# Optimization experiments

Measured on AMD Instinct MI355X. Metric: run time of the kernel, lower is better.

Reference implementation:

```python
import jax, jax.numpy as jnp
import numpy as np
from jax import lax

CORRKS = 7
EPS_CORR = 1e-6
EPS_IN = 1e-5
FLOW_SCALE = 1.0


def _gauss_kernel2d():
    # kornia get_gaussian_kernel1d(7, 1.5), separable -> outer product
    x = np.arange(7, dtype=np.float32) - 3.0
    g = np.exp(-(x ** 2) / (2.0 * 1.5 ** 2))
    g = g / g.sum()
    return jnp.asarray(np.outer(g, g), dtype=jnp.float32)  # [7,7]


def conv2d(x, w, b=None, padding=1, dilation=1, groups=1):
    y = lax.conv_general_dilated(
        x, w, window_strides=(1, 1),
        padding=[(padding, padding), (padding, padding)],
        rhs_dilation=(dilation, dilation),
        dimension_numbers=("NCHW", "OIHW", "NCHW"),
        feature_group_count=groups)
    if b is not None:
        y = y + b[None, :, None, None]
    return y


def gaussian_blur(x):
    # replicate padding then depthwise 7x7 gaussian conv
    c = x.shape[1]
    k2 = _gauss_kernel2d()
    w = jnp.broadcast_to(k2[None, None], (c, 1, 7, 7))
    xp = jnp.pad(x, ((0, 0), (0, 0), (3, 3), (3, 3)), mode="edge")
    return conv2d(xp, w, padding=0, groups=c)


def instance_norm(x, gamma, beta):
    mu = x.mean(axis=(2, 3), keepdims=True)
    var = x.var(axis=(2, 3), keepdims=True)
    xn = (x - mu) * lax.rsqrt(var + EPS_IN)
    return xn * gamma[None, :, None, None] + beta[None, :, None, None]


def lrelu(x):
    return jnp.where(x >= 0, x, 0.2 * x)


def nan0(x):
    return jnp.nan_to_num(x, nan=0.0, posinf=0.0, neginf=0.0)


def setup_inputs() -> dict:
    key = jax.random.key(0)
    ks = jax.random.split(key, 20)
    b, c, h, w = 4, 64, 256, 256

    def rn(k, shape, scale):
        return jax.random.normal(k, shape, dtype=jnp.float32) * scale

    d = {}
    d["feat1"] = rn(ks[0], (b, c, h, w), 1.0)
    d["feat2"] = rn(ks[1], (b, c, h, w), 1.0)
    # preprocessor: Conv(c, c, 3, pad=1), bias, no norm/act
    d["pre_w"] = rn(ks[2], (c, c, 3, 3), 0.05)
    d["pre_b"] = jnp.zeros((c,), jnp.float32)
    # featcompressor layer1: Conv(2c,2c,3), IN affine + LeakyReLU (no bias)
    d["fc1_w"] = rn(ks[3], (2 * c, 2 * c, 3, 3), 0.05)
    d["fc1_g"] = jnp.ones((2 * c,), jnp.float32)
    d["fc1_be"] = jnp.zeros((2 * c,), jnp.float32)
    # featcompressor layer2: Conv(2c,c,3), bias, no norm/act
    d["fc2_w"] = rn(ks[4], (c, 2 * c, 3, 3), 0.05)
    d["fc2_b"] = jnp.zeros((c,), jnp.float32)
    # estimator: (c+49)->64 d1, 64->32 d2, 32->16 d4; IN + LeakyReLU, no bias
    d["e1_w"] = rn(ks[5], (64, c + CORRKS * CORRKS, 3, 3), 0.05)
    d["e1_g"] = jnp.ones((64,), jnp.float32)
    d["e1_be"] = jnp.zeros((64,), jnp.float32)
    d["e2_w"] = rn(ks[6], (32, 64, 3, 3), 0.05)
    d["e2_g"] = jnp.ones((32,), jnp.float32)
    d["e2_be"] = jnp.zeros((32,), jnp.float32)
    d["e3_w"] = rn(ks[7], (16, 32, 3, 3), 0.05)
    d["e3_g"] = jnp.ones((16,), jnp.float32)
    d["e3_be"] = jnp.zeros((16,), jnp.float32)
    # flow head (torch zero-inits; use small random so output is non-degenerate)
    d["head_w"] = rn(ks[8], (2, 16, 3, 3), 0.05)
    d["head_b"] = jnp.zeros((2,), jnp.float32)
    return d


def reference(feat1, feat2, pre_w, pre_b, fc1_w, fc1_g, fc1_be, fc2_w, fc2_b,
              e1_w, e1_g, e1_be, e2_w, e2_g, e2_be, e3_w, e3_g, e3_be,
              head_w, head_b):
    # preprocessor applied to both features (cat on batch == apply separately)
    f1 = conv2d(feat1, pre_w, pre_b, padding=1)
    f2 = conv2d(feat2, pre_w, pre_b, padding=1)

    # featcompressor
    feat = conv2d(jnp.concatenate([f1, f2], axis=1), fc1_w, padding=1)
    feat = lrelu(instance_norm(feat, fc1_g, fc1_be))
    feat = conv2d(feat, fc2_w, fc2_b, padding=1)

    # local correlation: (feat2 - shifted blurred feat1)^2 mean over channels
    b, c, h, w = f2.shape
    f1s = gaussian_blur(f1)
    pad = CORRKS // 2  # corr_dilation=1
    f1p = jnp.pad(f1s, ((0, 0), (0, 0), (pad, pad), (pad, pad)))  # zero pad (F.unfold)
    lc = jnp.stack(
        [((f2 - f1p[:, :, i:i + h, j:j + w]) ** 2).mean(axis=1)
         for i in range(CORRKS) for j in range(CORRKS)], axis=1)  # [b,49,h,w]
    lc = lc / (lc.mean(axis=(1, 2, 3), keepdims=True) + EPS_CORR)
    corr = nan0(jnp.concatenate([feat, lc], axis=1))  # [b, c+49, h, w]

    # dilated conv estimator stack
    x = lrelu(instance_norm(conv2d(corr, e1_w, padding=1, dilation=1), e1_g, e1_be))
    x = lrelu(instance_norm(conv2d(x, e2_w, padding=2, dilation=2), e2_g, e2_be))
    x = lrelu(instance_norm(conv2d(x, e3_w, padding=4, dilation=4), e3_g, e3_be))

    disp = conv2d(x, head_w, head_b, padding=1) * FLOW_SCALE
    disp = nan0(gaussian_blur(disp))
    return disp
```

## Files before the change

kernel.cpp:

```cpp
#include <hip/hip_runtime.h>
#include <hip/hip_bf16.h>


typedef __attribute__((ext_vector_type(8))) short short8;
typedef __attribute__((ext_vector_type(4))) float f32x4;
typedef _Float16 f16x8 __attribute__((ext_vector_type(8)));
typedef _Float16 f16x2 __attribute__((ext_vector_type(2)));

__device__ __forceinline__ float s2f(short s) {
    unsigned int u = ((unsigned int)(unsigned short)s) << 16;
    float f; __builtin_memcpy(&f, &u, 4); return f;
}
__device__ __forceinline__ short f2s(float f) {
    __hip_bfloat16 h = __float2bfloat16(f);
    short s; __builtin_memcpy(&s, &h, 2); return s;
}
__device__ __forceinline__ float h2f(short s) {
    _Float16 h; __builtin_memcpy(&h, &s, 2); return (float)h;
}
__device__ __forceinline__ short f2h(float f) {
    _Float16 h = (_Float16)f;
    short s; __builtin_memcpy(&s, &h, 2); return s;
}

__device__ __forceinline__ float gw(int j) {
    const float G[7] = {0.0366329f, 0.1112808f, 0.2167453f, 0.2706821f,
                        0.2167453f, 0.1112808f, 0.0366329f};
    return G[j];
}

__global__ __launch_bounds__(256) void transpose_k(const float* __restrict__ in,
                                                   short* __restrict__ out)
{
    __shared__ float t[64][65];
    const int b = blockIdx.y;
    const int px0 = blockIdx.x * 64;
    #pragma unroll
    for (int k = 0; k < 16; ++k) {
        int idx = threadIdx.x + k * 256;
        int c = idx >> 6, x = idx & 63;
        t[c][x] = in[(size_t)(b * 64 + c) * 65536 + px0 + x];
    }
    __syncthreads();
    #pragma unroll
    for (int k = 0; k < 16; ++k) {
        int idx = threadIdx.x + k * 256;
        int px = idx >> 6, c = idx & 63;
        out[(size_t)(b * 65536 + px0 + px) * 64 + c] = f2s(t[c][px]);
    }
}

__global__ __launch_bounds__(256) void repack2_k(const float* __restrict__ w,
                                                 short* __restrict__ o,
                                                 int cout, int cin, int CINP)
{
    int idx = blockIdx.x * 256 + threadIdx.x;
    int CB = CINP >> 5;
    int tot = cout * 9 * CINP;
    if (idx >= tot) return;
    int c8   = idx & 7;
    int lane = (idx >> 3) & 63;
    int rest = idx >> 9;
    int cb   = rest % CB;
    int rest2 = rest / CB;
    int tap  = rest2 % 9;
    int o16  = rest2 / 9;
    int n16 = lane & 15, q = lane >> 4;
    int oc = o16 * 16 + n16;
    int ic = cb * 32 + q * 8 + c8;
    float v = (ic < cin) ? w[(size_t)(oc * cin + ic) * 9 + tap] : 0.f;
    o[idx] = f2s(v);
}

template<int DIL, int CINP, int WX, int WY, int NOC, int G>
__global__ __launch_bounds__(256) void convmfma_k(
    const short* __restrict__ srcA, const short* __restrict__ srcB,
    int splitK, int csA, int csB,
    const short* __restrict__ wgt, const float* __restrict__ bias,
    short* __restrict__ out, int OSTR, int OBASE, int b0)
{
    static_assert(WX * WY == 4, "4 waves per block");
    constexpr int PXW = G * 16;
    constexpr int PXB = PXW * WX;
    constexpr int XT  = 256 / PXB;
    constexpr int CB  = CINP / 32;
    constexpr int UQ  = CINP / 8;
    constexpr int UPX = UQ + 1;
    constexpr int WPX = PXB + 2 * DIL;

    __shared__ __align__(16) short lds[WPX * UPX * 8];

    const int tid  = threadIdx.x;
    const int lane = tid & 63;
    const int wave = tid >> 6;
    const int q = lane >> 4, n16 = lane & 15;
    const int wx = wave % WX, wy = wave / WX;

    constexpr int NX = XT * 256;
    const int bx = blockIdx.x;
    const int xs = (bx & 7) * (NX >> 3) + (bx >> 3);
    const int xt = xs % XT;
    const int y  = xs / XT;

    const int b  = b0 + blockIdx.z;
    const int ocWaveBase = blockIdx.y * (16 * NOC * WY) + wy * (16 * NOC);
    const int o16base = ocWaveBase >> 4;
    const int x0 = xt * PXB + wx * PXW;
    const int gxbase = xt * PXB - DIL;

    f32x4 acc[G][NOC];
    #pragma unroll
    for (int g = 0; g < G; ++g)
        #pragma unroll
        for (int t = 0; t < NOC; ++t)
            acc[g][t] = {0.f, 0.f, 0.f, 0.f};

    for (int dyi = 0; dyi < 3; ++dyi) {
        const int yy = y + (dyi - 1) * DIL;
        const bool rowok = ((unsigned)yy < 256u);
        __syncthreads();
        if (rowok) {
            const int rowbase = (b * 256 + yy) * 256;
            for (int i = tid; i < WPX * UQ; i += 256) {
                const int pxl = i / UQ;
                const int u   = i - pxl * UQ;
                const int gx  = gxbase + pxl;
                short8 v = {0, 0, 0, 0, 0, 0, 0, 0};
                if ((unsigned)gx < 256u) {
                    const int ic = u * 8;
                    const short* p = (ic < splitK)
                        ? srcA + (size_t)(rowbase + gx) * csA + ic
                        : srcB + (size_t)(rowbase + gx) * csB + (ic - splitK);
                    v = *reinterpret_cast<const short8*>(p);
                }
                *reinterpret_cast<short8*>(&lds[(pxl * UPX + u) * 8]) = v;
            }
        }
        __syncthreads();
        if (!rowok) continue;

        #pragma unroll
        for (int dxi = 0; dxi < 3; ++dxi) {
            const int tap = dyi * 3 + dxi;
            #pragma unroll
            for (int cb = 0; cb < CB; ++cb) {
                short8 bfr[G];
                #pragma unroll
                for (int g = 0; g < G; ++g) {
                    const int pxl = wx * PXW + g * 16 + n16 + dxi * DIL;
                    bfr[g] = *reinterpret_cast<const short8*>(
                        &lds[(pxl * UPX + cb * 4 + q) * 8]);
                }
                #pragma unroll
                for (int t = 0; t < NOC; ++t) {
                    short8 a = *reinterpret_cast<const short8*>(
                        wgt + ((((size_t)(o16base + t) * 9 + tap) * CB + cb) * 64 + lane) * 8);
                    #pragma unroll
                    for (int g = 0; g < G; ++g)
                        acc[g][t] = __builtin_amdgcn_mfma_f32_16x16x32_bf16(
                            a, bfr[g], acc[g][t], 0, 0, 0);
                }
            }
        }
    }

    #pragma unroll
    for (int g = 0; g < G; ++g) {
        const size_t px_lin = (size_t)(b * 256 + y) * 256 + x0 + g * 16 + n16;
        #pragma unroll
        for (int t = 0; t < NOC; ++t) {
            const int oc = ocWaveBase + t * 16 + q * 4;
            f32x4 v = acc[g][t];
            if (bias) {
                v.x += bias[oc];     v.y += bias[oc + 1];
                v.z += bias[oc + 2]; v.w += bias[oc + 3];
            }
            ushort4 pk;
            pk.x = (unsigned short)f2s(v.x);
            pk.y = (unsigned short)f2s(v.y);
            pk.z = (unsigned short)f2s(v.z);
            pk.w = (unsigned short)f2s(v.w);
            *reinterpret_cast<ushort4*>(out + px_lin * OSTR + OBASE + oc) = pk;
        }
    }
}

__global__ __launch_bounds__(256) void in_stats_nhwc_k(const short* __restrict__ x,
                                                       float* __restrict__ sums,
                                                       int C, int lC)
{
    __shared__ float ls[256], lss[256];
    const int tid = threadIdx.x;
    const int b = blockIdx.y;
    const int c = tid & (C - 1);
    const int sub = tid >> lC;
    const int tpc = 256 >> lC;
    const int px0 = blockIdx.x * 512;
    float s = 0.f, ss = 0.f;
    for (int p = sub; p < 512; p += tpc) {
        float v = s2f(x[(size_t)(b * 65536 + px0 + p) * C + c]);
        s += v; ss += v * v;
    }
    ls[tid] = s; lss[tid] = ss;
    __syncthreads();
    if (tid < C) {
        float s0 = ls[tid], ss0 = lss[tid];
        for (int j = 1; j < tpc; ++j) { s0 += ls[tid + j * C]; ss0 += lss[tid + j * C]; }
        atomicAdd(sums + 2 * (b * C + tid), s0);
        atomicAdd(sums + 2 * (b * C + tid) + 1, ss0);
    }
}

__global__ __launch_bounds__(256) void in_finalize_k(const float* __restrict__ sums,
                                                     float* __restrict__ stats, int n)
{
    int i = blockIdx.x * 256 + threadIdx.x;
    if (i >= n) return;
    float m = sums[2 * i] * (1.f / 65536.f);
    float var = sums[2 * i + 1] * (1.f / 65536.f) - m * m;
    if (var < 0.f) var = 0.f;
    stats[2 * i] = m;
    stats[2 * i + 1] = rsqrtf(var + 1e-5f);
}

__global__ __launch_bounds__(256) void in_apply_nhwc_k(short* __restrict__ x,
                                                       const float* __restrict__ stats,
                                                       const float* __restrict__ gamma,
                                                       const float* __restrict__ beta,
                                                       int C, int lC, int n4)
{
    int i = blockIdx.x * 256 + threadIdx.x;
    if (i >= n4) return;
    int e0 = i * 4;
    int c0 = e0 & (C - 1);
    int b = e0 >> (16 + lC);
    ushort4 u = reinterpret_cast<ushort4*>(x)[i];
    unsigned short vs[4] = {u.x, u.y, u.z, u.w};
    #pragma unroll
    for (int j = 0; j < 4; ++j) {
        int bc = b * C + c0 + j;
        float t = (s2f((short)vs[j]) - stats[2 * bc]) * stats[2 * bc + 1]
                  * gamma[c0 + j] + beta[c0 + j];
        vs[j] = (unsigned short)f2s(t >= 0.f ? t : 0.2f * t);
    }
    u.x = vs[0]; u.y = vs[1]; u.z = vs[2]; u.w = vs[3];
    reinterpret_cast<ushort4*>(x)[i] = u;
}

__global__ __launch_bounds__(256) void blur_k(const short* __restrict__ A,
                                              short* __restrict__ B1)
{
    __shared__ __align__(16) short raw[484 * 8];
    __shared__ __align__(16) float hb[352 * 12];

    const int tid  = threadIdx.x;
    const int tile = blockIdx.x >> 3;
    const int g    = blockIdx.x & 7;
    const int c0   = g * 8;
    const int tx = (tile & 15) << 4;
    const int ty = (tile >> 4) << 4;
    const int b  = blockIdx.y;

    #pragma unroll
    for (int it = 0; it < 2; ++it) {
        int i = tid + it * 256;
        if (i < 484) {
            int y = i / 22, x = i - y * 22;
            int gy = ty + y - 3, gx = tx + x - 3;
            gy = gy < 0 ? 0 : (gy > 255 ? 255 : gy);
            gx = gx < 0 ? 0 : (gx > 255 ? 255 : gx);
            *reinterpret_cast<short8*>(&raw[i * 8]) =
                *reinterpret_cast<const short8*>(
                    &A[(size_t)((b << 16) + (gy << 8) + gx) * 128 + c0]);
        }
    }
    __syncthreads();

    #pragma unroll
    for (int it = 0; it < 2; ++it) {
        int i = tid + it * 256;
        if (i < 352) {
            int r = i >> 4, cc = i & 15;
            float s[8];
            #pragma unroll
            for (int c = 0; c < 8; ++c) s[c] = 0.f;
            #pragma unroll
            for (int j = 0; j < 7; ++j) {
                short8 v = *reinterpret_cast<const short8*>(&raw[(r * 22 + cc + j) * 8]);
                float w = gw(j);
                #pragma unroll
                for (int c = 0; c < 8; ++c) s[c] += w * s2f(v[c]);
            }
            #pragma unroll
            for (int c = 0; c < 8; ++c) hb[i * 12 + c] = s[c];
        }
    }
    __syncthreads();

    const int py = tid >> 4, px = tid & 15;
    float s[8];
    #pragma unroll
    for (int c = 0; c < 8; ++c) s[c] = 0.f;
    #pragma unroll
    for (int j = 0; j < 7; ++j) {
        const float* hp = &hb[((py + j) * 16 + px) * 12];
        float w = gw(j);
        #pragma unroll
        for (int c = 0; c < 8; ++c) s[c] += w * hp[c];
    }
    short8 ov;
    #pragma unroll
    for (int c = 0; c < 8; ++c) ov[c] = f2h(s[c]);
    *reinterpret_cast<short8*>(
        &B1[(size_t)(((g * 4 + b) << 16) + ((ty + py) << 8) + tx + px) * 8]) = ov;
}

__global__ __launch_bounds__(256, 2) void corr2_k(const short* __restrict__ A,
                                                  const short* __restrict__ B1,
                                                  short* __restrict__ lcPad,
                                                  float* __restrict__ lcsum)
{
    __shared__ __align__(16) short blh[2][484 * 8];
    __shared__ float red[4];

    const int tid = threadIdx.x;
    const int tx = (blockIdx.x & 15) << 4;
    const int ty = (blockIdx.x >> 4) << 4;
    const int b  = blockIdx.y;
    const int py = tid >> 4, px = tid & 15;

    int y0 = tid / 22, x0c = tid - y0 * 22;
    int gy0 = ty + y0 - 3, gx0 = tx + x0c - 3;
    const bool ok0 = (gy0 >= 0 && gy0 < 256 && gx0 >= 0 && gx0 < 256);
    gy0 = gy0 < 0 ? 0 : (gy0 > 255 ? 255 : gy0);
    gx0 = gx0 < 0 ? 0 : (gx0 > 255 ? 255 : gx0);
    const int off0 = (gy0 << 8) + gx0;

    const int c1 = tid + 256;
    int y1 = c1 / 22, x1c = c1 - y1 * 22;
    int gy1 = ty + y1 - 3, gx1 = tx + x1c - 3;
    const bool ok1 = (gy1 >= 0 && gy1 < 256 && gx1 >= 0 && gx1 < 256);
    gy1 = gy1 < 0 ? 0 : (gy1 > 255 ? 255 : gy1);
    gx1 = gx1 < 0 ? 0 : (gx1 > 255 ? 255 : gx1);
    const int off1 = (gy1 << 8) + gx1;
    const bool has1 = (c1 < 484);

    const short* f2p = &A[(size_t)((b << 16) + ((ty + py) << 8) + tx + px) * 128 + 64];

    float acc[49];
    #pragma unroll
    for (int k = 0; k < 49; ++k) acc[k] = 0.f;

    for (int g = 0; g < 8; ++g) {
        const size_t plane = (size_t)(g * 4 + b) << 16;
        short* buf = blh[g & 1];

        {
            short8 v = *reinterpret_cast<const short8*>(&B1[(plane + off0) * 8]);
            if (!ok0) v = v ^ v;
            *reinterpret_cast<short8*>(&buf[tid * 8]) = v;
            if (has1) {
                short8 w = *reinterpret_cast<const short8*>(&B1[(plane + off1) * 8]);
                if (!ok1) w = w ^ w;
                *reinterpret_cast<short8*>(&buf[c1 * 8]) = w;
            }
        }

        short8 f2raw = *reinterpret_cast<const short8*>(f2p + g * 8);
        f16x8 f2v;
        #pragma unroll
        for (int c = 0; c < 8; ++c) f2v[c] = (_Float16)s2f(f2raw[c]);

        __syncthreads();

        const short* blp = &buf[(py * 22 + px) * 8];
        #pragma unroll
        for (int i = 0; i < 7; ++i)
            #pragma unroll
            for (int j = 0; j < 7; ++j) {
                f16x8 bv = *reinterpret_cast<const f16x8*>(blp + (i * 22 + j) * 8);
                f16x8 d = f2v - bv;
                float a = acc[i * 7 + j];
#if __has_builtin(__builtin_amdgcn_fdot2)
                a = __builtin_amdgcn_fdot2(__builtin_shufflevector(d, d, 0, 1),
                                           __builtin_shufflevector(d, d, 0, 1), a, false);
                a = __builtin_amdgcn_fdot2(__builtin_shufflevector(d, d, 2, 3),
                                           __builtin_shufflevector(d, d, 2, 3), a, false);
                a = __builtin_amdgcn_fdot2(__builtin_shufflevector(d, d, 4, 5),
                                           __builtin_shufflevector(d, d, 4, 5), a, false);
                a = __builtin_amdgcn_fdot2(__builtin_shufflevector(d, d, 6, 7),
                                           __builtin_shufflevector(d, d, 6, 7), a, false);
#else
                #pragma unroll
                for (int c = 0; c < 8; ++c) {
                    float df = (float)d[c];
                    a += df * df;
                }
#endif
                acc[i * 7 + j] = a;
            }
    }

    const size_t base = (size_t)((b << 16) + ((ty + py) << 8) + tx + px) * 64;
    float tot = 0.f;
    #pragma unroll
    for (int k = 0; k < 49; ++k) {
        float m = acc[k] * (1.f / 64.f);
        lcPad[base + k] = f2s(m);
        tot += m;
    }
    #pragma unroll
    for (int k = 49; k < 64; ++k) lcPad[base + k] = 0;

    for (int o = 32; o; o >>= 1) tot += __shfl_down(tot, o);
    if ((tid & 63) == 0) red[tid >> 6] = tot;
    __syncthreads();
    if (tid == 0) atomicAdd(lcsum + b, red[0] + red[1] + red[2] + red[3]);
}

__global__ __launch_bounds__(256) void lc_norm_k(short* __restrict__ lc,
                                                 const float* __restrict__ ls, int n4)
{
    int i = blockIdx.x * 256 + threadIdx.x;
    if (i >= n4) return;
    int b = (i * 4) >> 22;
    float sc = 1.f / (ls[b] * (1.f / 3211264.f) + 1e-6f);
    ushort4 u = reinterpret_cast<ushort4*>(lc)[i];
    u.x = (unsigned short)f2s(s2f((short)u.x) * sc);
    u.y = (unsigned short)f2s(s2f((short)u.y) * sc);
    u.z = (unsigned short)f2s(s2f((short)u.z) * sc);
    u.w = (unsigned short)f2s(s2f((short)u.w) * sc);
    reinterpret_cast<ushort4*>(lc)[i] = u;
}

__global__ __launch_bounds__(256) void head_k(const short* __restrict__ e3,
                                              const float* __restrict__ w,
                                              const float* __restrict__ bias,
                                              float* __restrict__ hd)
{
    int pix = blockIdx.x * 256 + threadIdx.x;
    int b = pix >> 16, rem = pix & 65535;
    int y = rem >> 8, x = rem & 255;
    float a0 = bias[0], a1 = bias[1];
    #pragma unroll
    for (int tap = 0; tap < 9; ++tap) {
        int yy = y + tap / 3 - 1, xx = x + tap % 3 - 1;
        if ((unsigned)yy >= 256u || (unsigned)xx >= 256u) continue;
        const short* p = e3 + (size_t)((b << 16) + (yy << 8) + xx) * 16;
        #pragma unroll
        for (int ic = 0; ic < 16; ++ic) {
            float v = s2f(p[ic]);
            a0 += v * w[ic * 9 + tap];
            a1 += v * w[(16 + ic) * 9 + tap];
        }
    }
    hd[(size_t)(b * 2) * 65536 + rem]     = a0;
    hd[(size_t)(b * 2 + 1) * 65536 + rem] = a1;
}

__global__ __launch_bounds__(256) void blur7f_k(const float* __restrict__ in,
                                                float* __restrict__ out)
{
    __shared__ float raw[22 * 22];
    __shared__ float hb[22 * 16];
    const int tid = threadIdx.x;
    const int tx = (blockIdx.x & 15) << 4;
    const int ty = (blockIdx.x >> 4) << 4;
    const size_t ch = ((size_t)blockIdx.y) << 16;
    const int py = tid >> 4, px = tid & 15;

    for (int i = tid; i < 484; i += 256) {
        int y = i / 22, x = i - y * 22;
        int gy = ty + y - 3, gx = tx + x - 3;
        gy = gy < 0 ? 0 : (gy > 255 ? 255 : gy);
        gx = gx < 0 ? 0 : (gx > 255 ? 255 : gx);
        raw[i] = in[ch + (gy << 8) + gx];
    }
    __syncthreads();
    for (int i = tid; i < 352; i += 256) {
        int r = i >> 4, cc = i & 15;
        float s = 0.f;
        #pragma unroll
        for (int j = 0; j < 7; ++j) s += gw(j) * raw[r * 22 + cc + j];
        hb[i] = s;
    }
    __syncthreads();
    float s = 0.f;
    #pragma unroll
    for (int j = 0; j < 7; ++j) s += gw(j) * hb[(py + j) * 16 + px];
    out[ch + ((ty + py) << 8) + tx + px] = s;
}

extern "C" void kernel_launch(void* const* d_in, const int* in_sizes, int n_in,
                              void* d_out, int out_size, void* d_ws, size_t ws_size,
                              hipStream_t stream)
{
    const float* feat1  = (const float*)d_in[0];
    const float* feat2  = (const float*)d_in[1];
    const float* pre_w  = (const float*)d_in[2];
    const float* pre_b  = (const float*)d_in[3];
    const float* fc1_w  = (const float*)d_in[4];
    const float* fc1_g  = (const float*)d_in[5];
    const float* fc1_be = (const float*)d_in[6];
    const float* fc2_w  = (const float*)d_in[7];
    const float* fc2_b  = (const float*)d_in[8];
    const float* e1_w   = (const float*)d_in[9];
    const float* e1_g   = (const float*)d_in[10];
    const float* e1_be  = (const float*)d_in[11];
    const float* e2_w   = (const float*)d_in[12];
    const float* e2_g   = (const float*)d_in[13];
    const float* e2_be  = (const float*)d_in[14];
    const float* e3_w   = (const float*)d_in[15];
    const float* e3_g   = (const float*)d_in[16];
    const float* e3_be  = (const float*)d_in[17];
    const float* head_w = (const float*)d_in[18];
    const float* head_b = (const float*)d_in[19];
    float* out = (float*)d_out;

    const size_t NEED = 152000000;
    if (ws_size < NEED) return;

    char* ws = (char*)d_ws;
    short* T1      = (short*)(ws);
    short* T2      = (short*)(ws + 33554432);
    short* lcPad   = (short*)(ws);
    short* B1h     = (short*)(ws + 33554432);
    short* featBuf = (short*)(ws + 33554432);
    short* A       = (short*)(ws + 67108864);
    short* FC1o    = (short*)(ws + 83886080);
    short* E1o     = (short*)(ws + 67108864);
    short* E2o     = (short*)(ws + 100663296);
    short* E3o     = (short*)(ws + 117440512);
    float* HD      = (float*)(ws + 125829120);
    short* preW    = (short*)(ws + 150994944);
    short* fc1W    = (short*)(ws + 151068672);
    short* fc2W    = (short*)(ws + 151363584);
    short* e1W     = (short*)(ws + 151511040);
    short* e2W     = (short*)(ws + 151658496);
    short* e3W     = (short*)(ws + 151695360);
    float* sums0   = (float*)(ws + 151704576);
    float* sums1   = (float*)(ws + 151708672);
    float* sums2   = (float*)(ws + 151712768);
    float* sums3   = (float*)(ws + 151716864);
    float* stats0  = (float*)(ws + 151720960);
    float* stats1  = (float*)(ws + 151725056);
    float* stats2  = (float*)(ws + 151729152);
    float* stats3  = (float*)(ws + 151733248);
    float* LS      = (float*)(ws + 151737344);

    hipMemsetAsync(ws + 151704576, 0, 32784, stream);

    transpose_k<<<dim3(1024, 4), 256, 0, stream>>>(feat1, T1);
    transpose_k<<<dim3(1024, 4), 256, 0, stream>>>(feat2, T2);

    repack2_k<<<144, 256, 0, stream>>>(pre_w, preW, 64, 64, 64);
    repack2_k<<<576, 256, 0, stream>>>(fc1_w, fc1W, 128, 128, 128);
    repack2_k<<<288, 256, 0, stream>>>(fc2_w, fc2W, 64, 128, 128);
    repack2_k<<<288, 256, 0, stream>>>(e1_w, e1W, 64, 113, 128);
    repack2_k<<<72, 256, 0, stream>>>(e2_w, e2W, 32, 64, 64);
    repack2_k<<<18, 256, 0, stream>>>(e3_w, e3W, 16, 32, 32);

    convmfma_k<1, 64, 2, 2, 2, 4><<<dim3(512, 1, 4), 256, 0, stream>>>(
        T1, T1, 64, 64, 64, preW, pre_b, A, 128, 0, 0);
    convmfma_k<1, 64, 2, 2, 2, 4><<<dim3(512, 1, 4), 256, 0, stream>>>(
        T2, T2, 64, 64, 64, preW, pre_b, A, 128, 64, 0);

    blur_k<<<dim3(2048, 4), 256, 0, stream>>>(A, B1h);
    corr2_k<<<dim3(256, 4), 256, 0, stream>>>(A, B1h, lcPad, LS);
    lc_norm_k<<<16384, 256, 0, stream>>>(lcPad, LS, 4194304);

    for (int b = 3; b >= 0; --b)
        convmfma_k<1, 128, 2, 2, 4, 4><<<dim3(512, 1, 1), 256, 0, stream>>>(
            A, A, 128, 128, 128, fc1W, nullptr, FC1o, 128, 0, b);
    in_stats_nhwc_k<<<dim3(128, 4), 256, 0, stream>>>(FC1o, sums0, 128, 7);
    in_finalize_k<<<2, 256, 0, stream>>>(sums0, stats0, 512);
    in_apply_nhwc_k<<<32768, 256, 0, stream>>>(FC1o, stats0, fc1_g, fc1_be, 128, 7, 8388608);

    convmfma_k<1, 128, 2, 2, 2, 4><<<dim3(512, 1, 4), 256, 0, stream>>>(
        FC1o, FC1o, 128, 128, 128, fc2W, fc2_b, featBuf, 64, 0, 0);

    convmfma_k<1, 128, 2, 2, 2, 4><<<dim3(512, 1, 4), 256, 0, stream>>>(
        featBuf, lcPad, 64, 64, 64, e1W, nullptr, E1o, 64, 0, 0);
    in_stats_nhwc_k<<<dim3(128, 4), 256, 0, stream>>>(E1o, sums1, 64, 6);
    in_finalize_k<<<1, 256, 0, stream>>>(sums1, stats1, 256);
    in_apply_nhwc_k<<<16384, 256, 0, stream>>>(E1o, stats1, e1_g, e1_be, 64, 6, 4194304);

    convmfma_k<2, 64, 2, 2, 1, 4><<<dim3(512, 1, 4), 256, 0, stream>>>(
        E1o, E1o, 64, 64, 64, e2W, nullptr, E2o, 32, 0, 0);
    in_stats_nhwc_k<<<dim3(128, 4), 256, 0, stream>>>(E2o, sums2, 32, 5);
    in_finalize_k<<<1, 256, 0, stream>>>(sums2, stats2, 128);
    in_apply_nhwc_k<<<8192, 256, 0, stream>>>(E2o, stats2, e2_g, e2_be, 32, 5, 2097152);

    convmfma_k<4, 32, 4, 1, 1, 4><<<dim3(256, 1, 4), 256, 0, stream>>>(
        E2o, E2o, 32, 32, 32, e3W, nullptr, E3o, 16, 0, 0);
    in_stats_nhwc_k<<<dim3(128, 4), 256, 0, stream>>>(E3o, sums3, 16, 4);
    in_finalize_k<<<1, 256, 0, stream>>>(sums3, stats3, 64);
    in_apply_nhwc_k<<<4096, 256, 0, stream>>>(E3o, stats3, e3_g, e3_be, 16, 4, 1048576);

    head_k<<<1024, 256, 0, stream>>>(E3o, head_w, head_b, HD);
    blur7f_k<<<dim3(256, 8), 256, 0, stream>>>(HD, out);
}
```

Before: 987.7 us.

## Fuse instance-norm apply and corr normalization into next conv's load path

Removes the standalone in_apply and lc_norm elementwise passes. The finalize kernel now folds gamma, beta, mean and rstd into a per-channel scale and shift. The consuming conv (or head) applies the affine plus LeakyReLU, or the lc scale, as it loads its input tile. The corr kernel also pads its LDS row stride to 24 and adds a trailing barrier between the double-buffered iterations. This saves several full read-modify-write passes over large bf16 activations, at the cost of extra global stats loads and ALU work in each conv's tile load, repeated for overlapping halo rows.

```diff
diff --git a/kernel.cpp b/kernel.cpp
--- a/kernel.cpp
+++ b/kernel.cpp
@@ -5,7 +5,6 @@
 typedef __attribute__((ext_vector_type(8))) short short8;
 typedef __attribute__((ext_vector_type(4))) float f32x4;
 typedef _Float16 f16x8 __attribute__((ext_vector_type(8)));
-typedef _Float16 f16x2 __attribute__((ext_vector_type(2)));
 
 __device__ __forceinline__ float s2f(short s) {
     unsigned int u = ((unsigned int)(unsigned short)s) << 16;
@@ -14,9 +13,6 @@
 __device__ __forceinline__ short f2s(float f) {
     __hip_bfloat16 h = __float2bfloat16(f);
     short s; __builtin_memcpy(&s, &h, 2); return s;
-}
-__device__ __forceinline__ float h2f(short s) {
-    _Float16 h; __builtin_memcpy(&h, &s, 2); return (float)h;
 }
 __device__ __forceinline__ short f2h(float f) {
     _Float16 h = (_Float16)f;
@@ -72,12 +68,13 @@
     o[idx] = f2s(v);
 }
 
-template<int DIL, int CINP, int WX, int WY, int NOC, int G>
+template<int DIL, int CINP, int WX, int WY, int NOC, int G, int MODE>
 __global__ __launch_bounds__(256) void convmfma_k(
     const short* __restrict__ srcA, const short* __restrict__ srcB,
     int splitK, int csA, int csB,
     const short* __restrict__ wgt, const float* __restrict__ bias,
-    short* __restrict__ out, int OSTR, int OBASE, int b0)
+    short* __restrict__ out, int OSTR, int OBASE, int b0,
+    const float* __restrict__ xf)
 {
     static_assert(WX * WY == 4, "4 waves per block");
     constexpr int PXW = G * 16;
@@ -107,6 +104,9 @@
     const int o16base = ocWaveBase >> 4;
     const int x0 = xt * PXB + wx * PXW;
     const int gxbase = xt * PXB - DIL;
+
+    const int bC = b * CINP;
+    const float sc = (MODE == 2) ? 1.f / (xf[b] * (1.f / 3211264.f) + 1e-6f) : 0.f;
 
     f32x4 acc[G][NOC];
     #pragma unroll
@@ -132,6 +132,22 @@
                         ? srcA + (size_t)(rowbase + gx) * csA + ic
                         : srcB + (size_t)(rowbase + gx) * csB + (ic - splitK);
                     v = *reinterpret_cast<const short8*>(p);
+                    if (MODE == 1) {
+                        #pragma unroll
+                        for (int c = 0; c < 8; ++c) {
+                            const float ka = xf[2 * (bC + ic + c)];
+                            const float kb = xf[2 * (bC + ic + c) + 1];
+                            float t = s2f(v[c]) * ka + kb;
+                            t = fmaxf(t, 0.2f * t);
+                            v[c] = f2s(t);
+                        }
+                    } else if (MODE == 2) {
+                        if (ic >= splitK) {
+                            #pragma unroll
+                            for (int c = 0; c < 8; ++c)
+                                v[c] = f2s(s2f(v[c]) * sc);
+                        }
+                    }
                 }
                 *reinterpret_cast<short8*>(&lds[(pxl * UPX + u) * 8]) = v;
             }
@@ -212,39 +228,20 @@
 }
 
 __global__ __launch_bounds__(256) void in_finalize_k(const float* __restrict__ sums,
-                                                     float* __restrict__ stats, int n)
+                                                     float* __restrict__ stats,
+                                                     const float* __restrict__ gamma,
+                                                     const float* __restrict__ beta,
+                                                     int lC, int n)
 {
     int i = blockIdx.x * 256 + threadIdx.x;
     if (i >= n) return;
+    int c = i & ((1 << lC) - 1);
     float m = sums[2 * i] * (1.f / 65536.f);
     float var = sums[2 * i + 1] * (1.f / 65536.f) - m * m;
     if (var < 0.f) var = 0.f;
-    stats[2 * i] = m;
-    stats[2 * i + 1] = rsqrtf(var + 1e-5f);
-}
-
-__global__ __launch_bounds__(256) void in_apply_nhwc_k(short* __restrict__ x,
-                                                       const float* __restrict__ stats,
-                                                       const float* __restrict__ gamma,
-                                                       const float* __restrict__ beta,
-                                                       int C, int lC, int n4)
-{
-    int i = blockIdx.x * 256 + threadIdx.x;
-    if (i >= n4) return;
-    int e0 = i * 4;
-    int c0 = e0 & (C - 1);
-    int b = e0 >> (16 + lC);
-    ushort4 u = reinterpret_cast<ushort4*>(x)[i];
-    unsigned short vs[4] = {u.x, u.y, u.z, u.w};
-    #pragma unroll
-    for (int j = 0; j < 4; ++j) {
-        int bc = b * C + c0 + j;
-        float t = (s2f((short)vs[j]) - stats[2 * bc]) * stats[2 * bc + 1]
-                  * gamma[c0 + j] + beta[c0 + j];
-        vs[j] = (unsigned short)f2s(t >= 0.f ? t : 0.2f * t);
-    }
-    u.x = vs[0]; u.y = vs[1]; u.z = vs[2]; u.w = vs[3];
-    reinterpret_cast<ushort4*>(x)[i] = u;
+    float ka = rsqrtf(var + 1e-5f) * gamma[c];
+    stats[2 * i] = ka;
+    stats[2 * i + 1] = beta[c] - m * ka;
 }
 
 __global__ __launch_bounds__(256) void blur_k(const short* __restrict__ A,
@@ -320,7 +317,7 @@
                                                   short* __restrict__ lcPad,
                                                   float* __restrict__ lcsum)
 {
-    __shared__ __align__(16) short blh[2][484 * 8];
+    __shared__ __align__(16) short blh[2][22 * 24 * 8];
     __shared__ float red[4];
 
     const int tid = threadIdx.x;
@@ -335,6 +332,7 @@
     gy0 = gy0 < 0 ? 0 : (gy0 > 255 ? 255 : gy0);
     gx0 = gx0 < 0 ? 0 : (gx0 > 255 ? 255 : gx0);
     const int off0 = (gy0 << 8) + gx0;
+    const int lc0 = y0 * 24 + x0c;
 
     const int c1 = tid + 256;
     int y1 = c1 / 22, x1c = c1 - y1 * 22;
@@ -343,6 +341,7 @@
     gy1 = gy1 < 0 ? 0 : (gy1 > 255 ? 255 : gy1);
     gx1 = gx1 < 0 ? 0 : (gx1 > 255 ? 255 : gx1);
     const int off1 = (gy1 << 8) + gx1;
+    const int lc1 = y1 * 24 + x1c;
     const bool has1 = (c1 < 484);
 
     const short* f2p = &A[(size_t)((b << 16) + ((ty + py) << 8) + tx + px) * 128 + 64];
@@ -358,11 +357,11 @@
         {
             short8 v = *reinterpret_cast<const short8*>(&B1[(plane + off0) * 8]);
             if (!ok0) v = v ^ v;
-            *reinterpret_cast<short8*>(&buf[tid * 8]) = v;
+            *reinterpret_cast<short8*>(&buf[lc0 * 8]) = v;
             if (has1) {
                 short8 w = *reinterpret_cast<const short8*>(&B1[(plane + off1) * 8]);
                 if (!ok1) w = w ^ w;
-                *reinterpret_cast<short8*>(&buf[c1 * 8]) = w;
+                *reinterpret_cast<short8*>(&buf[lc1 * 8]) = w;
             }
         }
 
@@ -373,12 +372,12 @@
 
         __syncthreads();
 
-        const short* blp = &buf[(py * 22 + px) * 8];
+        const short* blp = &buf[(py * 24 + px) * 8];
         #pragma unroll
         for (int i = 0; i < 7; ++i)
             #pragma unroll
             for (int j = 0; j < 7; ++j) {
-                f16x8 bv = *reinterpret_cast<const f16x8*>(blp + (i * 22 + j) * 8);
+                f16x8 bv = *reinterpret_cast<const f16x8*>(blp + (i * 24 + j) * 8);
                 f16x8 d = f2v - bv;
                 float a = acc[i * 7 + j];
 #if __has_builtin(__builtin_amdgcn_fdot2)
@@ -399,6 +398,7 @@
 #endif
                 acc[i * 7 + j] = a;
             }
+        __syncthreads();
     }
 
     const size_t base = (size_t)((b << 16) + ((ty + py) << 8) + tx + px) * 64;
@@ -418,29 +418,21 @@
     if (tid == 0) atomicAdd(lcsum + b, red[0] + red[1] + red[2] + red[3]);
 }
 
-__global__ __launch_bounds__(256) void lc_norm_k(short* __restrict__ lc,
-                                                 const float* __restrict__ ls, int n4)
-{
-    int i = blockIdx.x * 256 + threadIdx.x;
-    if (i >= n4) return;
-    int b = (i * 4) >> 22;
-    float sc = 1.f / (ls[b] * (1.f / 3211264.f) + 1e-6f);
-    ushort4 u = reinterpret_cast<ushort4*>(lc)[i];
-    u.x = (unsigned short)f2s(s2f((short)u.x) * sc);
-    u.y = (unsigned short)f2s(s2f((short)u.y) * sc);
-    u.z = (unsigned short)f2s(s2f((short)u.z) * sc);
-    u.w = (unsigned short)f2s(s2f((short)u.w) * sc);
-    reinterpret_cast<ushort4*>(lc)[i] = u;
-}
-
 __global__ __launch_bounds__(256) void head_k(const short* __restrict__ e3,
                                               const float* __restrict__ w,
                                               const float* __restrict__ bias,
+                                              const float* __restrict__ kst,
                                               float* __restrict__ hd)
 {
     int pix = blockIdx.x * 256 + threadIdx.x;
     int b = pix >> 16, rem = pix & 65535;
     int y = rem >> 8, x = rem & 255;
+    float ka[16], kb[16];
+    #pragma unroll
+    for (int ic = 0; ic < 16; ++ic) {
+        ka[ic] = kst[2 * (b * 16 + ic)];
+        kb[ic] = kst[2 * (b * 16 + ic) + 1];
+    }
     float a0 = bias[0], a1 = bias[1];
     #pragma unroll
     for (int tap = 0; tap < 9; ++tap) {
@@ -449,7 +441,8 @@
         const short* p = e3 + (size_t)((b << 16) + (yy << 8) + xx) * 16;
         #pragma unroll
         for (int ic = 0; ic < 16; ++ic) {
-            float v = s2f(p[ic]);
+            float v = s2f(p[ic]) * ka[ic] + kb[ic];
+            v = fmaxf(v, 0.2f * v);
             a0 += v * w[ic * 9 + tap];
             a1 += v * w[(16 + ic) * 9 + tap];
         }
@@ -560,43 +553,38 @@
     repack2_k<<<72, 256, 0, stream>>>(e2_w, e2W, 32, 64, 64);
     repack2_k<<<18, 256, 0, stream>>>(e3_w, e3W, 16, 32, 32);
 
-    convmfma_k<1, 64, 2, 2, 2, 4><<<dim3(512, 1, 4), 256, 0, stream>>>(
-        T1, T1, 64, 64, 64, preW, pre_b, A, 128, 0, 0);
-    convmfma_k<1, 64, 2, 2, 2, 4><<<dim3(512, 1, 4), 256, 0, stream>>>(
-        T2, T2, 64, 64, 64, preW, pre_b, A, 128, 64, 0);
+    convmfma_k<1, 64, 2, 2, 2, 4, 0><<<dim3(512, 1, 4), 256, 0, stream>>>(
+        T1, T1, 64, 64, 64, preW, pre_b, A, 128, 0, 0, nullptr);
+    convmfma_k<1, 64, 2, 2, 2, 4, 0><<<dim3(512, 1, 4), 256, 0, stream>>>(
+        T2, T2, 64, 64, 64, preW, pre_b, A, 128, 64, 0, nullptr);
 
     blur_k<<<dim3(2048, 4), 256, 0, stream>>>(A, B1h);
     corr2_k<<<dim3(256, 4), 256, 0, stream>>>(A, B1h, lcPad, LS);
-    lc_norm_k<<<16384, 256, 0, stream>>>(lcPad, LS, 4194304);
 
     for (int b = 3; b >= 0; --b)
-        convmfma_k<1, 128, 2, 2, 4, 4><<<dim3(512, 1, 1), 256, 0, stream>>>(
-            A, A, 128, 128, 128, fc1W, nullptr, FC1o, 128, 0, b);
+        convmfma_k<1, 128, 2, 2, 4, 4, 0><<<dim3(512, 1, 1), 256, 0, stream>>>(
+            A, A, 128, 128, 128, fc1W, nullptr, FC1o, 128, 0, b, nullptr);
     in_stats_nhwc_k<<<dim3(128, 4), 256, 0, stream>>>(FC1o, sums0, 128, 7);
-    in_finalize_k<<<2, 256, 0, stream>>>(sums0, stats0, 512);
-    in_apply_nhwc_k<<<32768, 256, 0, stream>>>(FC1o, stats0, fc1_g, fc1_be, 128, 7, 8388608);
-
-    convmfma_k<1, 128, 2, 2, 2, 4><<<dim3(512, 1, 4), 256, 0, stream>>>(
-        FC1o, FC1o, 128, 128, 128, fc2W, fc2_b, featBuf, 64, 0, 0);
-
-    convmfma_k<1, 128, 2, 2, 2, 4><<<dim3(512, 1, 4), 256, 0, stream>>>(
-        featBuf, lcPad, 64, 64, 64, e1W, nullptr, E1o, 64, 0, 0);
+    in_finalize_k<<<2, 256, 0, stream>>>(sums0, stats0, fc1_g, fc1_be, 7, 512);
+
+    convmfma_k<1, 128, 2, 2, 2, 4, 1><<<dim3(512, 1, 4), 256, 0, stream>>>(
+        FC1o, FC1o, 128, 128, 128, fc2W, fc2_b, featBuf, 64, 0, 0, stats0);
+
+    convmfma_k<1, 128, 2, 2, 2, 4, 2><<<dim3(512, 1, 4), 256, 0, stream>>>(
+        featBuf, lcPad, 64, 64, 64, e1W, nullptr, E1o, 64, 0, 0, LS);
     in_stats_nhwc_k<<<dim3(128, 4), 256, 0, stream>>>(E1o, sums1, 64, 6);
-    in_finalize_k<<<1, 256, 0, stream>>>(sums1, stats1, 256);
-    in_apply_nhwc_k<<<16384, 256, 0, stream>>>(E1o, stats1, e1_g, e1_be, 64, 6, 4194304);
-
-    convmfma_k<2, 64, 2, 2, 1, 4><<<dim3(512, 1, 4), 256, 0, stream>>>(
-        E1o, E1o, 64, 64, 64, e2W, nullptr, E2o, 32, 0, 0);
+    in_finalize_k<<<1, 256, 0, stream>>>(sums1, stats1, e1_g, e1_be, 6, 256);
+
+    convmfma_k<2, 64, 2, 2, 1, 4, 1><<<dim3(512, 1, 4), 256, 0, stream>>>(
+        E1o, E1o, 64, 64, 64, e2W, nullptr, E2o, 32, 0, 0, stats1);
     in_stats_nhwc_k<<<dim3(128, 4), 256, 0, stream>>>(E2o, sums2, 32, 5);
-    in_finalize_k<<<1, 256, 0, stream>>>(sums2, stats2, 128);
-    in_apply_nhwc_k<<<8192, 256, 0, stream>>>(E2o, stats2, e2_g, e2_be, 32, 5, 2097152);
-
-    convmfma_k<4, 32, 4, 1, 1, 4><<<dim3(256, 1, 4), 256, 0, stream>>>(
-        E2o, E2o, 32, 32, 32, e3W, nullptr, E3o, 16, 0, 0);
+    in_finalize_k<<<1, 256, 0, stream>>>(sums2, stats2, e2_g, e2_be, 5, 128);
+
+    convmfma_k<4, 32, 4, 1, 1, 4, 1><<<dim3(256, 1, 4), 256, 0, stream>>>(
+        E2o, E2o, 32, 32, 32, e3W, nullptr, E3o, 16, 0, 0, stats2);
     in_stats_nhwc_k<<<dim3(128, 4), 256, 0, stream>>>(E3o, sums3, 16, 4);
-    in_finalize_k<<<1, 256, 0, stream>>>(sums3, stats3, 64);
-    in_apply_nhwc_k<<<4096, 256, 0, stream>>>(E3o, stats3, e3_g, e3_be, 16, 4, 1048576);
-
-    head_k<<<1024, 256, 0, stream>>>(E3o, head_w, head_b, HD);
+    in_finalize_k<<<1, 256, 0, stream>>>(sums3, stats3, e3_g, e3_be, 4, 64);
+
+    head_k<<<1024, 256, 0, stream>>>(E3o, head_w, head_b, stats3, HD);
     blur7f_k<<<dim3(256, 8), 256, 0, stream>>>(HD, out);
 }
```

After: 965.6 us. 2.2% less time.
